# Optimization experiments

Hardware: AMD Instinct MI355X
Metric: run time of the kernel (lower is better)

Reference implementation:

```python
import jax, jax.numpy as jnp
import numpy as np

B, M, K, N = 4, 2048, 4096, 4096


def setup_inputs() -> dict:
    key = jax.random.key(0)
    k1, k2, k3, k4, k5 = jax.random.split(key, 5)
    # int8 quantized activations and weights (stored as int8, like the torch buffers)
    x_q = jax.random.randint(k1, (B, M, K), -128, 127, dtype=jnp.int8)
    weight = jax.random.randint(k2, (N, K), -128, 127, dtype=jnp.int8)
    # per-token activation scales and per-output-row weight scales (symmetric quant)
    scales_x = jax.random.uniform(k3, (B, M, 1), dtype=jnp.float32) * 0.01 + 1e-4
    weight_scales = jax.random.uniform(k4, (N, 1), dtype=jnp.float32) * 0.01 + 1e-4
    bias = jax.random.normal(k5, (N,), dtype=jnp.float32)
    return {"x_q": x_q, "scales_x": scales_x, "weight": weight,
            "weight_scales": weight_scales, "bias": bias}


def reference(x_q, scales_x, weight, weight_scales, bias):
    # int8 GEMM accumulating in int32: (B*M, K) @ (K, N) with weight stored (N, K)
    acc = jnp.einsum(
        'bmk,nk->bmn',
        x_q.astype(jnp.int32), weight.astype(jnp.int32),
        preferred_element_type=jnp.int32,
    )  # [B, M, N] int32
    # symmetric dequant: row (token) scale * column (output-channel) scale, then bias
    out = acc.astype(jnp.float32) * scales_x * weight_scales[:, 0] + bias
    return out.astype(jnp.float16)
```

## Files before the change

kernel.cpp:

```cpp
#include <hip/hip_runtime.h>

typedef int v4i __attribute__((ext_vector_type(4)));

constexpr int Kdim = 4096;
constexpr int Ndim = 4096;
constexpr int MtotC = 8192;
constexpr int BM = 256;
constexpr int BN = 256;
constexpr int NH = 64;

#define AS1 __attribute__((address_space(1)))
#define AS3 __attribute__((address_space(3)))

__global__ void pack_i32_to_i8(const int* __restrict__ xq, const int* __restrict__ wq,
                               signed char* __restrict__ x8, signed char* __restrict__ w8,
                               size_t nx4, size_t nw4) {
    size_t i = (size_t)blockIdx.x * blockDim.x + threadIdx.x;
    size_t stride = (size_t)gridDim.x * blockDim.x;
    size_t tot = nx4 + nw4;
    for (size_t j = i; j < tot; j += stride) {
        if (j < nx4) {
            const int4 v = ((const int4*)xq)[j];
            char4 c;
            c.x = (signed char)v.x; c.y = (signed char)v.y;
            c.z = (signed char)v.z; c.w = (signed char)v.w;
            ((char4*)x8)[j] = c;
        } else {
            const size_t k = j - nx4;
            const int4 v = ((const int4*)wq)[k];
            char4 c;
            c.x = (signed char)v.x; c.y = (signed char)v.y;
            c.z = (signed char)v.z; c.w = (signed char)v.w;
            ((char4*)w8)[k] = c;
        }
    }
}

__global__ __launch_bounds__(512, 2) void i8gemm_kernel(
    const signed char* __restrict__ A,
    const signed char* __restrict__ W,
    const float* __restrict__ sx,
    const float* __restrict__ wsc,
    const float* __restrict__ bias,
    float* __restrict__ C)
{
    extern __shared__ signed char smem[];

    const int tid  = threadIdx.x;
    const int wave = tid >> 6;
    const int lane = tid & 63;
    const int wr = wave >> 2;
    const int wc = wave & 3;

    const int xr_ = blockIdx.x & 7;
    const int idx = blockIdx.x >> 3;
    const int bm = ((xr_ & 3) * 8 + (idx & 7)) * BM;
    const int bn = ((xr_ >> 2) * 8 + (idx >> 3)) * BN;

    const int srow  = tid >> 2;
    const int gslot = (tid & 3) ^ ((srow >> 1) & 3);
    const signed char* Ag = A + (size_t)(bm + srow) * Kdim + gslot * 16;
    const signed char* Wg = W + (size_t)(bn + srow) * Kdim + gslot * 16;
    const int sdst = srow * 64 + (tid & 3) * 16;

    const int frow = lane & 15;
    const int fsl  = lane >> 4;
    const int rsw  = ((fsl ^ ((frow >> 1) & 3)) << 4);
    const int aro  = (wr * 128 + frow) * 64 + rsw;
    const int bro  = 16384 + (wc * 64 + frow) * 64 + rsw;

    v4i acc[8][4];
#pragma unroll
    for (int f = 0; f < 8; ++f)
#pragma unroll
        for (int g = 0; g < 4; ++g)
#pragma unroll
            for (int e = 0; e < 4; ++e) acc[f][g][e] = 0;

    v4i avA[8], bvA[4], avB[8], bvB[4];

#define REG_OF(M) ((((M) >> 1) & 1) * 65536 + ((M) & 1) * 32768)

#define STG_HALF(M) do {                                                               \
    signed char* dst = smem + REG_OF(M) + sdst;                                        \
    const signed char* sa = Ag + (size_t)(M) * 64;                                     \
    const signed char* sb = Wg + (size_t)(M) * 64;                                     \
    __builtin_amdgcn_global_load_lds((const AS1 void*)sa,                        (AS3 void*)dst,           16, 0, 0); \
    __builtin_amdgcn_global_load_lds((const AS1 void*)(sa + (size_t)128 * Kdim), (AS3 void*)(dst + 8192),  16, 0, 0); \
    __builtin_amdgcn_global_load_lds((const AS1 void*)sb,                        (AS3 void*)(dst + 16384), 16, 0, 0); \
    __builtin_amdgcn_global_load_lds((const AS1 void*)(sb + (size_t)128 * Kdim), (AS3 void*)(dst + 24576), 16, 0, 0); \
} while (0)

#define READ_SET(AV, BV, M) do {                                                       \
    const signed char* base_ = smem + REG_OF(M);                                       \
    _Pragma("unroll") for (int g_ = 0; g_ < 4; ++g_)                                   \
        BV[g_] = *(const v4i*)(base_ + bro + g_ * 1024);                               \
    _Pragma("unroll") for (int f_ = 0; f_ < 8; ++f_)                                   \
        AV[f_] = *(const v4i*)(base_ + aro + f_ * 1024);                               \
} while (0)

#define MFMA_SET(AV, BV) do {                                                          \
    __builtin_amdgcn_s_setprio(1);                                                     \
    _Pragma("unroll") for (int f_ = 0; f_ < 8; ++f_)                                   \
    _Pragma("unroll") for (int g_ = 0; g_ < 4; ++g_)                                   \
        acc[f_][g_] = __builtin_amdgcn_mfma_i32_16x16x64_i8(AV[f_], BV[g_], acc[f_][g_], 0, 0, 0); \
    __builtin_amdgcn_s_setprio(0);                                                     \
} while (0)

#define BAR     __builtin_amdgcn_s_barrier()
#define LGKM12  do { asm volatile("s_waitcnt lgkmcnt(12)" ::: "memory");               \
                     __builtin_amdgcn_sched_barrier(0); } while (0)
#define LGKM0   do { asm volatile("s_waitcnt lgkmcnt(0)" ::: "memory");                \
                     __builtin_amdgcn_sched_barrier(0); } while (0)
#define VMC(N)  asm volatile("s_waitcnt vmcnt(" #N ")" ::: "memory")

    STG_HALF(0);
    STG_HALF(1);
    STG_HALF(2);
    VMC(8);
    BAR;
    READ_SET(avA, bvA, 0);

    for (int u = 0; u < 30; ++u) {
        const int q = 2 * u;
        VMC(4);
        BAR;
        STG_HALF(q + 3);
        READ_SET(avB, bvB, q + 1);
        LGKM12;
        MFMA_SET(avA, bvA);
        VMC(4);
        BAR;
        STG_HALF(q + 4);
        READ_SET(avA, bvA, q + 2);
        LGKM12;
        MFMA_SET(avB, bvB);
    }

    VMC(4);
    BAR;
    STG_HALF(63);
    READ_SET(avB, bvB, 61);
    LGKM12;
    MFMA_SET(avA, bvA);
    VMC(4);
    BAR;
    READ_SET(avA, bvA, 62);
    LGKM12;
    MFMA_SET(avB, bvB);

    VMC(0);
    BAR;
    READ_SET(avB, bvB, 63);
    LGKM12;
    MFMA_SET(avA, bvA);
    LGKM0;
    MFMA_SET(avB, bvB);

    const int orow0 = bm + wr * 128;
    const int ocol0 = bn + wc * 64;
    float wsv[4], bvv[4];
#pragma unroll
    for (int g = 0; g < 4; ++g) {
        const int col = ocol0 + g * 16 + frow;
        wsv[g] = wsc[col];
        bvv[g] = bias[col];
    }
#pragma unroll
    for (int f = 0; f < 8; ++f) {
#pragma unroll
        for (int jr = 0; jr < 4; ++jr) {
            const int row = orow0 + f * 16 + fsl * 4 + jr;
            const float s = sx[row];
#pragma unroll
            for (int g = 0; g < 4; ++g) {
                const int col = ocol0 + g * 16 + frow;
                C[(size_t)row * Ndim + col] = (float)acc[f][g][jr] * s * wsv[g] + bvv[g];
            }
        }
    }
#undef REG_OF
#undef STG_HALF
#undef READ_SET
#undef MFMA_SET
#undef BAR
#undef LGKM12
#undef LGKM0
#undef VMC
}

extern "C" void kernel_launch(void* const* d_in, const int* in_sizes, int n_in,
                              void* d_out, int out_size, void* d_ws, size_t ws_size,
                              hipStream_t stream) {
    (void)in_sizes; (void)n_in; (void)out_size; (void)ws_size;
    const int*   x_q  = (const int*)d_in[0];
    const float* sx   = (const float*)d_in[1];
    const int*   w_q  = (const int*)d_in[2];
    const float* wsc  = (const float*)d_in[3];
    const float* bias = (const float*)d_in[4];
    float* out = (float*)d_out;

    signed char* x8 = (signed char*)d_ws;
    signed char* w8 = x8 + (size_t)MtotC * Kdim;

    const size_t nx = (size_t)MtotC * Kdim;
    const size_t nw = (size_t)Ndim * Kdim;

    pack_i32_to_i8<<<3072, 256, 0, stream>>>(x_q, w_q, x8, w8, nx / 4, nw / 4);

    static bool attr_set = false;
    if (!attr_set) {
        hipFuncSetAttribute((const void*)i8gemm_kernel,
                            hipFuncAttributeMaxDynamicSharedMemorySize, 131072);
        attr_set = true;
    }

    const int nwg = (MtotC / BM) * (Ndim / BN);
    i8gemm_kernel<<<nwg, 512, 131072, stream>>>(x8, w8, sx, wsc, bias, out);
}
```

Measured before the change: 188.1 us.

## Pre-swizzle weights into MFMA fragment layout and load B directly to registers

The pack kernel now writes the int8 weight into a per-64-column-strip layout that matches the MFMA B-fragment lane order. The GEMM kernel loads B fragments straight from global memory into registers, skipping LDS staging, and keeps only A in LDS (64 KB static instead of 128 KB dynamic). This cuts LDS traffic and footprint. The cost is that every wave re-reads B from global or L2 with no LDS sharing, and global-load latency now sits on the MFMA critical path behind the vmcnt waits.

```diff
diff --git a/kernel.cpp b/kernel.cpp
--- a/kernel.cpp
+++ b/kernel.cpp
@@ -7,44 +7,57 @@
 constexpr int MtotC = 8192;
 constexpr int BM = 256;
 constexpr int BN = 256;
-constexpr int NH = 64;
 
 #define AS1 __attribute__((address_space(1)))
 #define AS3 __attribute__((address_space(3)))
 
-__global__ void pack_i32_to_i8(const int* __restrict__ xq, const int* __restrict__ wq,
-                               signed char* __restrict__ x8, signed char* __restrict__ w8,
-                               size_t nx4, size_t nw4) {
-    size_t i = (size_t)blockIdx.x * blockDim.x + threadIdx.x;
-    size_t stride = (size_t)gridDim.x * blockDim.x;
-    size_t tot = nx4 + nw4;
-    for (size_t j = i; j < tot; j += stride) {
-        if (j < nx4) {
+__global__ void pack_both(const int* __restrict__ xq, const int* __restrict__ wq,
+                          signed char* __restrict__ x8, signed char* __restrict__ w8t) {
+    const size_t gid = (size_t)blockIdx.x * blockDim.x + threadIdx.x;
+    if (blockIdx.x < 2048) {
+        const size_t nx4 = (size_t)MtotC * Kdim / 4;
+        for (size_t j = gid; j < nx4; j += 524288) {
             const int4 v = ((const int4*)xq)[j];
             char4 c;
             c.x = (signed char)v.x; c.y = (signed char)v.y;
             c.z = (signed char)v.z; c.w = (signed char)v.w;
             ((char4*)x8)[j] = c;
-        } else {
-            const size_t k = j - nx4;
-            const int4 v = ((const int4*)wq)[k];
-            char4 c;
-            c.x = (signed char)v.x; c.y = (signed char)v.y;
-            c.z = (signed char)v.z; c.w = (signed char)v.w;
-            ((char4*)w8)[k] = c;
+        }
+    } else {
+        const size_t t2 = gid - (size_t)2048 * 256;
+        const size_t ng = (size_t)Ndim * (Kdim / 16);
+        for (size_t ggg = t2; ggg < ng; ggg += 131072) {
+            const int n   = (int)(ggg >> 8);
+            const int k16 = (int)(ggg & 255);
+            const int* src = wq + (size_t)n * Kdim + k16 * 16;
+            char4 c[4];
+#pragma unroll
+            for (int q = 0; q < 4; ++q) {
+                const int4 v = ((const int4*)src)[q];
+                c[q].x = (signed char)v.x; c[q].y = (signed char)v.y;
+                c[q].z = (signed char)v.z; c[q].w = (signed char)v.w;
+            }
+            const int strip = n >> 6, cw = n & 63;
+            const int g = cw >> 4, frow = cw & 15;
+            const int u = k16 >> 3, h = (k16 >> 2) & 1, fsl = k16 & 3;
+            const int lane = fsl * 16 + frow;
+            char4* dst = (char4*)(w8t + (size_t)strip * 262144 + u * 8192 + h * 4096
+                                  + g * 1024 + lane * 16);
+#pragma unroll
+            for (int q = 0; q < 4; ++q) dst[q] = c[q];
         }
     }
 }
 
 __global__ __launch_bounds__(512, 2) void i8gemm_kernel(
     const signed char* __restrict__ A,
-    const signed char* __restrict__ W,
+    const signed char* __restrict__ Bt,
     const float* __restrict__ sx,
     const float* __restrict__ wsc,
     const float* __restrict__ bias,
     float* __restrict__ C)
 {
-    extern __shared__ signed char smem[];
+    __shared__ signed char smem[65536];
 
     const int tid  = threadIdx.x;
     const int wave = tid >> 6;
@@ -60,14 +73,14 @@
     const int srow  = tid >> 2;
     const int gslot = (tid & 3) ^ ((srow >> 1) & 3);
     const signed char* Ag = A + (size_t)(bm + srow) * Kdim + gslot * 16;
-    const signed char* Wg = W + (size_t)(bn + srow) * Kdim + gslot * 16;
     const int sdst = srow * 64 + (tid & 3) * 16;
 
     const int frow = lane & 15;
     const int fsl  = lane >> 4;
     const int rsw  = ((fsl ^ ((frow >> 1) & 3)) << 4);
     const int aro  = (wr * 128 + frow) * 64 + rsw;
-    const int bro  = 16384 + (wc * 64 + frow) * 64 + rsw;
+
+    const signed char* Bw = Bt + ((size_t)(bn >> 6) + wc) * 262144 + lane * 16;
 
     v4i acc[8][4];
 #pragma unroll
@@ -77,29 +90,30 @@
 #pragma unroll
             for (int e = 0; e < 4; ++e) acc[f][g][e] = 0;
 
-    v4i avA[8], bvA[4], avB[8], bvB[4];
-
-#define REG_OF(M) ((((M) >> 1) & 1) * 65536 + ((M) & 1) * 32768)
-
-#define STG_HALF(M) do {                                                               \
+    v4i avA[8], avB[8], bv0[4], bv1[4];
+
+#define REG_OF(M) (((M) & 3) * 16384)
+
+#define STG_A(M) do {                                                                  \
     signed char* dst = smem + REG_OF(M) + sdst;                                        \
     const signed char* sa = Ag + (size_t)(M) * 64;                                     \
-    const signed char* sb = Wg + (size_t)(M) * 64;                                     \
-    __builtin_amdgcn_global_load_lds((const AS1 void*)sa,                        (AS3 void*)dst,           16, 0, 0); \
-    __builtin_amdgcn_global_load_lds((const AS1 void*)(sa + (size_t)128 * Kdim), (AS3 void*)(dst + 8192),  16, 0, 0); \
-    __builtin_amdgcn_global_load_lds((const AS1 void*)sb,                        (AS3 void*)(dst + 16384), 16, 0, 0); \
-    __builtin_amdgcn_global_load_lds((const AS1 void*)(sb + (size_t)128 * Kdim), (AS3 void*)(dst + 24576), 16, 0, 0); \
-} while (0)
-
-#define READ_SET(AV, BV, M) do {                                                       \
+    __builtin_amdgcn_global_load_lds((const AS1 void*)sa,                        (AS3 void*)dst,          16, 0, 0); \
+    __builtin_amdgcn_global_load_lds((const AS1 void*)(sa + (size_t)128 * Kdim), (AS3 void*)(dst + 8192), 16, 0, 0); \
+} while (0)
+
+#define B_LOAD(BV, M) do {                                                             \
+    const signed char* bsrc = Bw + (size_t)((M) >> 1) * 8192 + ((M) & 1) * 4096;       \
+    _Pragma("unroll") for (int g_ = 0; g_ < 4; ++g_)                                   \
+        BV[g_] = *(const v4i*)(bsrc + g_ * 1024);                                      \
+} while (0)
+
+#define READ_A(AV, M) do {                                                             \
     const signed char* base_ = smem + REG_OF(M);                                       \
-    _Pragma("unroll") for (int g_ = 0; g_ < 4; ++g_)                                   \
-        BV[g_] = *(const v4i*)(base_ + bro + g_ * 1024);                               \
     _Pragma("unroll") for (int f_ = 0; f_ < 8; ++f_)                                   \
         AV[f_] = *(const v4i*)(base_ + aro + f_ * 1024);                               \
 } while (0)
 
-#define MFMA_SET(AV, BV) do {                                                          \
+#define MFMA_HALF(AV, BV) do {                                                         \
     __builtin_amdgcn_s_setprio(1);                                                     \
     _Pragma("unroll") for (int f_ = 0; f_ < 8; ++f_)                                   \
     _Pragma("unroll") for (int g_ = 0; g_ < 4; ++g_)                                   \
@@ -107,55 +121,55 @@
     __builtin_amdgcn_s_setprio(0);                                                     \
 } while (0)
 
-#define BAR     __builtin_amdgcn_s_barrier()
-#define LGKM12  do { asm volatile("s_waitcnt lgkmcnt(12)" ::: "memory");               \
-                     __builtin_amdgcn_sched_barrier(0); } while (0)
-#define LGKM0   do { asm volatile("s_waitcnt lgkmcnt(0)" ::: "memory");                \
-                     __builtin_amdgcn_sched_barrier(0); } while (0)
-#define VMC(N)  asm volatile("s_waitcnt vmcnt(" #N ")" ::: "memory")
-
-    STG_HALF(0);
-    STG_HALF(1);
-    STG_HALF(2);
+#define BAR    __builtin_amdgcn_s_barrier()
+#define LGKM8  do { asm volatile("s_waitcnt lgkmcnt(8)" ::: "memory");                 \
+                    __builtin_amdgcn_sched_barrier(0); } while (0)
+#define LGKM0  do { asm volatile("s_waitcnt lgkmcnt(0)" ::: "memory");                 \
+                    __builtin_amdgcn_sched_barrier(0); } while (0)
+#define VMC(N) asm volatile("s_waitcnt vmcnt(" #N ")" ::: "memory")
+
+    STG_A(0);
+    STG_A(1);
+    B_LOAD(bv0, 0);
+    STG_A(2);
     VMC(8);
     BAR;
-    READ_SET(avA, bvA, 0);
+    READ_A(avA, 0);
 
     for (int u = 0; u < 30; ++u) {
-        const int q = 2 * u;
-        VMC(4);
-        BAR;
-        STG_HALF(q + 3);
-        READ_SET(avB, bvB, q + 1);
-        LGKM12;
-        MFMA_SET(avA, bvA);
-        VMC(4);
-        BAR;
-        STG_HALF(q + 4);
-        READ_SET(avA, bvA, q + 2);
-        LGKM12;
-        MFMA_SET(avB, bvB);
-    }
-
-    VMC(4);
-    BAR;
-    STG_HALF(63);
-    READ_SET(avB, bvB, 61);
-    LGKM12;
-    MFMA_SET(avA, bvA);
-    VMC(4);
-    BAR;
-    READ_SET(avA, bvA, 62);
-    LGKM12;
-    MFMA_SET(avB, bvB);
-
+        const int m = 2 * u;
+        VMC(2); BAR;
+        B_LOAD(bv1, m + 1);
+        STG_A(m + 3);
+        READ_A(avB, m + 1);
+        LGKM8;
+        MFMA_HALF(avA, bv0);
+        VMC(2); BAR;
+        B_LOAD(bv0, m + 2);
+        STG_A(m + 4);
+        READ_A(avA, m + 2);
+        LGKM8;
+        MFMA_HALF(avB, bv1);
+    }
+    VMC(2); BAR;
+    B_LOAD(bv1, 61);
+    STG_A(63);
+    READ_A(avB, 61);
+    LGKM8;
+    MFMA_HALF(avA, bv0);
+    VMC(2); BAR;
+    B_LOAD(bv0, 62);
+    READ_A(avA, 62);
+    LGKM8;
+    MFMA_HALF(avB, bv1);
+    VMC(0); BAR;
+    B_LOAD(bv1, 63);
+    READ_A(avB, 63);
+    LGKM8;
+    MFMA_HALF(avA, bv0);
     VMC(0);
-    BAR;
-    READ_SET(avB, bvB, 63);
-    LGKM12;
-    MFMA_SET(avA, bvA);
     LGKM0;
-    MFMA_SET(avB, bvB);
+    MFMA_HALF(avB, bv1);
 
     const int orow0 = bm + wr * 128;
     const int ocol0 = bn + wc * 64;
@@ -180,11 +194,12 @@
         }
     }
 #undef REG_OF
-#undef STG_HALF
-#undef READ_SET
-#undef MFMA_SET
+#undef STG_A
+#undef B_LOAD
+#undef READ_A
+#undef MFMA_HALF
 #undef BAR
-#undef LGKM12
+#undef LGKM8
 #undef LGKM0
 #undef VMC
 }
@@ -200,21 +215,11 @@
     const float* bias = (const float*)d_in[4];
     float* out = (float*)d_out;
 
-    signed char* x8 = (signed char*)d_ws;
-    signed char* w8 = x8 + (size_t)MtotC * Kdim;
-
-    const size_t nx = (size_t)MtotC * Kdim;
-    const size_t nw = (size_t)Ndim * Kdim;
-
-    pack_i32_to_i8<<<3072, 256, 0, stream>>>(x_q, w_q, x8, w8, nx / 4, nw / 4);
-
-    static bool attr_set = false;
-    if (!attr_set) {
-        hipFuncSetAttribute((const void*)i8gemm_kernel,
-                            hipFuncAttributeMaxDynamicSharedMemorySize, 131072);
-        attr_set = true;
-    }
+    signed char* x8  = (signed char*)d_ws;
+    signed char* w8t = x8 + (size_t)MtotC * Kdim;
+
+    pack_both<<<2560, 256, 0, stream>>>(x_q, w_q, x8, w8t);
 
     const int nwg = (MtotC / BM) * (Ndim / BN);
-    i8gemm_kernel<<<nwg, 512, 131072, stream>>>(x8, w8, sx, wsc, bias, out);
+    i8gemm_kernel<<<nwg, 512, 0, stream>>>(x8, w8t, sx, wsc, bias, out);
 }
```

After: 212.6 us. 13.0% more time.
